# Kernel optimization log

Measured on AMD Instinct MI355X. Metric: run time of the kernel, lower is better.

## Reference

```python
import jax, jax.numpy as jnp
import numpy as np

NUM_LANDMARKS = 256
PINV_ITERS = 6


def iterative_inv(K):
    # Newton-Schulz iterative pseudo-inverse (Nystromformer), K: [B, m, m]
    I = jnp.eye(K.shape[-1], dtype=K.dtype)
    V = K.swapaxes(-1, -2) / (jnp.max(jnp.sum(K, axis=-2)) * jnp.max(jnp.sum(K, axis=-1)))
    for _ in range(PINV_ITERS):
        KV = K @ V
        V = 0.25 * V @ (13.0 * I - KV @ (15.0 * I - KV @ (7.0 * I - KV)))
    return V


def nystrom_attention_matrix(q, k, m):
    # q, k: [B, N, d] -> approximate softmax(q k^T / sqrt(d)) of shape [B, N, N]
    B, N, d = q.shape
    scale = 1.0 / jnp.sqrt(jnp.asarray(d, q.dtype))
    L = N // m
    q_l = q.reshape(B, m, L, d).mean(axis=2)  # landmark queries [B, m, d]
    k_l = k.reshape(B, m, L, d).mean(axis=2)  # landmark keys    [B, m, d]
    k1 = jax.nn.softmax(jnp.einsum('bnd,bmd->bnm', q, k_l) * scale, axis=-1)   # [B, N, m]
    k2 = jax.nn.softmax(jnp.einsum('bld,bmd->blm', q_l, k_l) * scale, axis=-1) # [B, m, m]
    k3 = jax.nn.softmax(jnp.einsum('bmd,bnd->bmn', q_l, k) * scale, axis=-1)   # [B, m, N]
    return (k1 @ iterative_inv(k2)) @ k3  # [B, N, N]


def setup_inputs() -> dict:
    key = jax.random.key(0)
    ks = jax.random.split(key, 8)
    B, C, T, W, H = 2, 64, 4, 32, 32
    d = C // 8
    scale = 0.05  # keep q.k scores in a sane softmax range
    return {
        'x': jax.random.normal(ks[0], (B, C, T, W, H), dtype=jnp.float32),
        'wq': jax.random.normal(ks[1], (d, C), dtype=jnp.float32) * scale,
        'bq': jax.random.normal(ks[2], (d,), dtype=jnp.float32) * scale,
        'wk': jax.random.normal(ks[3], (d, C), dtype=jnp.float32) * scale,
        'bk': jax.random.normal(ks[4], (d,), dtype=jnp.float32) * scale,
        'wv': jax.random.normal(ks[5], (C, C), dtype=jnp.float32) * scale,
        'bv': jax.random.normal(ks[6], (C,), dtype=jnp.float32) * scale,
        'gamma': jax.random.normal(ks[7], (1,), dtype=jnp.float32),
    }


def reference(x, wq, bq, wk, bk, wv, bv, gamma):
    B, C, T, W, H = x.shape
    N = T * W * H
    xf = x.reshape(B, C, N)
    # 1x1x1 Conv3d == per-token linear over channels
    q = jnp.einsum('oc,bcn->bno', wq, xf) + bq            # [B, N, C//8]
    k = jnp.einsum('oc,bcn->bno', wk, xf) + bk            # [B, N, C//8]
    v = jnp.einsum('oc,bcn->bon', wv, xf) + bv[None, :, None]  # [B, C, N]
    attn = nystrom_attention_matrix(q, k, NUM_LANDMARKS)  # [B, N, N]
    # out = bmm(value, attn^T): out[b,c,i] = sum_j v[b,c,j] * attn[b,i,j]
    out = jnp.einsum('bcj,bij->bci', v, attn).reshape(B, C, T, W, H)
    out = gamma[0] * out + x
    return out, attn
```

## Files before the change

### kernel.cpp

```cpp
#include <hip/hip_runtime.h>
#include <hip/hip_bf16.h>
#include <math.h>

#define NB 2
#define NC 64
#define ND 8
#define NN 4096
#define NM 256
#define NL 16
#define SCALE 0.35355339059327373f
#define A_ROOT 4.1303956f
#define B_COEF (-2.8696044f)
#define C_COEF 3.1474086f

typedef __attribute__((ext_vector_type(4))) float f32x4;
typedef __attribute__((ext_vector_type(8))) short bf16x8;
typedef __attribute__((ext_vector_type(4))) short bf16x4;

__device__ inline ushort f2bf(float f) {
  __hip_bfloat16 h = __float2bfloat16(f);
  return *reinterpret_cast<ushort*>(&h);
}
__device__ inline float bf2f(ushort u) {
  return __uint_as_float(((unsigned int)u) << 16);
}

__device__ inline void gl_lds16(const void* g, void* l) {
  __builtin_amdgcn_global_load_lds(
      (const __attribute__((address_space(1))) unsigned int*)g,
      (__attribute__((address_space(3))) unsigned int*)l, 16, 0, 0);
}

__device__ inline unsigned lds_addr(const void* p) {
  return (unsigned)(size_t)(__attribute__((address_space(3))) const void*)p;
}

__global__ __launch_bounds__(256) void qkv2_kernel(
    const float* __restrict__ x,
    const float* __restrict__ wq, const float* __restrict__ bq,
    const float* __restrict__ wk, const float* __restrict__ bk,
    const float* __restrict__ wv, const float* __restrict__ bv,
    float* __restrict__ q, float* __restrict__ k, float* __restrict__ v) {
  __shared__ float ws[NC];
  int o = blockIdx.x;
  int b = blockIdx.z;
  int n0 = blockIdx.y * 1024;
  int t = threadIdx.x;
  const float* wrow;
  float bias;
  if (o < ND)            { wrow = wq + (size_t)o * NC;            bias = bq[o]; }
  else if (o < 2 * ND)   { wrow = wk + (size_t)(o - ND) * NC;     bias = bk[o - ND]; }
  else                   { wrow = wv + (size_t)(o - 2 * ND) * NC; bias = bv[o - 2 * ND]; }
  if (t < NC) ws[t] = wrow[t];
  __syncthreads();
  int n = n0 + t * 4;
  float4 acc = {bias, bias, bias, bias};
  #pragma unroll
  for (int c = 0; c < NC; ++c) {
    float wc = ws[c];
    float4 xv = *(const float4*)(x + ((size_t)b * NC + c) * NN + n);
    acc.x += wc * xv.x; acc.y += wc * xv.y; acc.z += wc * xv.z; acc.w += wc * xv.w;
  }
  if (o < ND) {
    float* qp = q + ((size_t)b * NN + n) * ND + o;
    qp[0] = acc.x; qp[8] = acc.y; qp[16] = acc.z; qp[24] = acc.w;
  } else if (o < 2 * ND) {
    float* kp = k + ((size_t)b * NN + n) * ND + (o - ND);
    kp[0] = acc.x; kp[8] = acc.y; kp[16] = acc.z; kp[24] = acc.w;
  } else {
    *(float4*)(v + ((size_t)b * NC + (o - 2 * ND)) * NN + n) = acc;
  }
}

__global__ void landmark_kernel(const float* __restrict__ q, const float* __restrict__ k,
                                float* __restrict__ ql, float* __restrict__ kl) {
  int idx = blockIdx.x * 256 + threadIdx.x;
  int b = idx / (NM * ND), r = idx % (NM * ND), i = r / ND, o = r % ND;
  float sq = 0.f, sk = 0.f;
  for (int l = 0; l < NL; ++l) {
    size_t base = ((size_t)b * NN + i * NL + l) * ND + o;
    sq += q[base]; sk += k[base];
  }
  ql[idx] = sq * (1.0f / NL);
  kl[idx] = sk * (1.0f / NL);
}

__global__ __launch_bounds__(256) void scores_softmax_m_bf16(
    const float* __restrict__ Q, int R, const float* __restrict__ KL,
    ushort* __restrict__ out) {
  __shared__ float skl[NM][9];
  int b = blockIdx.y;
  int t = threadIdx.x;
  for (int i = t; i < NM * ND; i += 256) skl[i >> 3][i & 7] = KL[(size_t)b * NM * ND + i];
  __syncthreads();
  int wave = t >> 6, lane = t & 63;
  int r = blockIdx.x * 4 + wave;
  const float* qrow = Q + ((size_t)b * R + r) * ND;
  float qr[ND];
  #pragma unroll
  for (int dd = 0; dd < ND; ++dd) qr[dd] = qrow[dd];
  float sc[4];
  float lmax = -1e30f;
  #pragma unroll
  for (int s = 0; s < 4; ++s) {
    int j = lane + 64 * s;
    float a = 0.f;
    #pragma unroll
    for (int dd = 0; dd < ND; ++dd) a += qr[dd] * skl[j][dd];
    sc[s] = a * SCALE;
    lmax = fmaxf(lmax, sc[s]);
  }
  for (int off = 32; off; off >>= 1) lmax = fmaxf(lmax, __shfl_xor(lmax, off));
  float lsum = 0.f;
  #pragma unroll
  for (int s = 0; s < 4; ++s) { sc[s] = expf(sc[s] - lmax); lsum += sc[s]; }
  for (int off = 32; off; off >>= 1) lsum += __shfl_xor(lsum, off);
  float inv = 1.0f / lsum;
  #pragma unroll
  for (int s = 0; s < 4; ++s)
    out[((size_t)b * R + r) * NM + lane + 64 * s] = f2bf(sc[s] * inv);
}

__global__ __launch_bounds__(256) void scores_softmax_m_f32(
    const float* __restrict__ Q, int R, const float* __restrict__ KL,
    float* __restrict__ out) {
  __shared__ float skl[NM][9];
  int b = blockIdx.y;
  int t = threadIdx.x;
  for (int i = t; i < NM * ND; i += 256) skl[i >> 3][i & 7] = KL[(size_t)b * NM * ND + i];
  __syncthreads();
  int wave = t >> 6, lane = t & 63;
  int r = blockIdx.x * 4 + wave;
  const float* qrow = Q + ((size_t)b * R + r) * ND;
  float qr[ND];
  #pragma unroll
  for (int dd = 0; dd < ND; ++dd) qr[dd] = qrow[dd];
  float sc[4];
  float lmax = -1e30f;
  #pragma unroll
  for (int s = 0; s < 4; ++s) {
    int j = lane + 64 * s;
    float a = 0.f;
    #pragma unroll
    for (int dd = 0; dd < ND; ++dd) a += qr[dd] * skl[j][dd];
    sc[s] = a * SCALE;
    lmax = fmaxf(lmax, sc[s]);
  }
  for (int off = 32; off; off >>= 1) lmax = fmaxf(lmax, __shfl_xor(lmax, off));
  float lsum = 0.f;
  #pragma unroll
  for (int s = 0; s < 4; ++s) { sc[s] = expf(sc[s] - lmax); lsum += sc[s]; }
  for (int off = 32; off; off >>= 1) lsum += __shfl_xor(lsum, off);
  float inv = 1.0f / lsum;
  #pragma unroll
  for (int s = 0; s < 4; ++s) out[((size_t)b * R + r) * NM + lane + 64 * s] = sc[s] * inv;
}

__global__ __launch_bounds__(256) void scores_softmax_n(
    const float* __restrict__ QL, const float* __restrict__ Kt,
    ushort* __restrict__ out) {
  __shared__ float wred[4], wsum[4];
  int b = blockIdx.y, i = blockIdx.x;
  int t = threadIdx.x;
  float qr[ND];
  #pragma unroll
  for (int dd = 0; dd < ND; ++dd) qr[dd] = QL[((size_t)b * NM + i) * ND + dd];
  float sc[16];
  float lmax = -1e30f;
  #pragma unroll
  for (int s = 0; s < 16; ++s) {
    int n = t + 256 * s;
    const float* kp = Kt + ((size_t)b * NN + n) * ND;
    float a = 0.f;
    #pragma unroll
    for (int dd = 0; dd < ND; ++dd) a += qr[dd] * kp[dd];
    sc[s] = a * SCALE;
    lmax = fmaxf(lmax, sc[s]);
  }
  for (int off = 32; off; off >>= 1) lmax = fmaxf(lmax, __shfl_xor(lmax, off));
  if ((t & 63) == 0) wred[t >> 6] = lmax;
  __syncthreads();
  lmax = fmaxf(fmaxf(wred[0], wred[1]), fmaxf(wred[2], wred[3]));
  float lsum = 0.f;
  #pragma unroll
  for (int s = 0; s < 16; ++s) { sc[s] = expf(sc[s] - lmax); lsum += sc[s]; }
  for (int off = 32; off; off >>= 1) lsum += __shfl_xor(lsum, off);
  if ((t & 63) == 0) wsum[t >> 6] = lsum;
  __syncthreads();
  lsum = wsum[0] + wsum[1] + wsum[2] + wsum[3];
  float inv = 1.0f / lsum;
  #pragma unroll
  for (int s = 0; s < 16; ++s)
    out[((size_t)b * NM + i) * NN + t + 256 * s] = f2bf(sc[s] * inv);
}

__global__ __launch_bounds__(256) void denom_kernel(const float* __restrict__ k2,
                                                    float* __restrict__ denw) {
  __shared__ float red[256];
  int b = blockIdx.x;
  int t = threadIdx.x;
  float cs = 0.f;
  for (int i = 0; i < NM; ++i) cs += k2[((size_t)b * NM + i) * NM + t];
  red[t] = cs;
  __syncthreads();
  for (int off = 128; off; off >>= 1) {
    if (t < off) red[t] = fmaxf(red[t], red[t + off]);
    __syncthreads();
  }
  if (t == 0) denw[b] = red[0];
}

__global__ void vinit_kernel(const float* __restrict__ k2, const float* __restrict__ denw,
                             float* __restrict__ V) {
  int idx = blockIdx.x * 256 + threadIdx.x;
  int b = idx / (NM * NM), r = idx % (NM * NM), i = r / NM, j = r % NM;
  float dval = 1.0f / fmaxf(denw[0], denw[1]);
  V[idx] = k2[((size_t)b * NM + j) * NM + i] * dval;
}

#define NS_SMEM 70144

__device__ __forceinline__ void ns_tile(
    const float* __restrict__ A, const float* __restrict__ B,
    const float* __restrict__ B2, float* __restrict__ O,
    float s_a, float s_ab, size_t bo, int bi, int bj, char* smem, int t) {
  typedef float ARow[260];
  typedef float BRow[36];
  ARow* As = (ARow*)smem;
  BRow* Bs = (BRow*)(smem + 33280);
  #pragma unroll
  for (int q = 0; q < 8; ++q) {
    int s = q * 256 + t;
    int ar = s >> 6, ac = (s & 63) * 4;
    *(float4*)&As[ar][ac] = *(const float4*)(A + bo + (size_t)(bi + ar) * NM + ac);
    int bk = s >> 3, bc = (s & 7) * 4;
    if (B2 == nullptr) {
      *(float4*)&Bs[bk][bc] = *(const float4*)(B + bo + (size_t)bk * NM + bj + bc);
    } else {
      float4 v = *(const float4*)(B + bo + (size_t)bk * NM + bj + bc);
      float4 z = *(const float4*)(B2 + bo + (size_t)bk * NM + bj + bc);
      float4 rr;
      rr.x = v.x + B_COEF * z.x; rr.y = v.y + B_COEF * z.y;
      rr.z = v.z + B_COEF * z.z; rr.w = v.w + B_COEF * z.w;
      int d = bk - bj - bc;
      if (d >= 0 && d < 4) ((float*)&rr)[d] += C_COEF;
      *(float4*)&Bs[bk][bc] = rr;
    }
  }
  __syncthreads();
  int tx = t & 15, ty = t >> 4;
  float acc[2][2] = {};
  #pragma unroll 8
  for (int kk = 0; kk < NM; ++kk) {
    float a0 = As[ty * 2][kk], a1 = As[ty * 2 + 1][kk];
    float b0 = Bs[kk][tx * 2], b1 = Bs[kk][tx * 2 + 1];
    acc[0][0] += a0 * b0; acc[0][1] += a0 * b1;
    acc[1][0] += a1 * b0; acc[1][1] += a1 * b1;
  }
  #pragma unroll
  for (int i = 0; i < 2; ++i)
    #pragma unroll
    for (int j = 0; j < 2; ++j) {
      size_t o = bo + (size_t)(bi + ty * 2 + i) * NM + bj + tx * 2 + j;
      float r = s_ab * acc[i][j];
      if (s_a != 0.0f) r += s_a * A[o];
      O[o] = r;
    }
}

__global__ __launch_bounds__(256) void ns_z_kernel(
    const float* __restrict__ k2, const float* __restrict__ V, float* __restrict__ Z) {
  __shared__ char smem[NS_SMEM];
  int blk = blockIdx.x, t = threadIdx.x;
  int b = blk >> 6, tile = blk & 63;
  int bi = (tile >> 3) * 32, bj = (tile & 7) * 32;
  ns_tile(k2, V, nullptr, Z, 0.f, 1.f, (size_t)b * NM * NM, bi, bj, smem, t);
}

__global__ __launch_bounds__(256) void ns_uz2_kernel(
    const float* __restrict__ V, const float* __restrict__ Z,
    float* __restrict__ U, float* __restrict__ Z2) {
  __shared__ char smem[NS_SMEM];
  int blk = blockIdx.x, t = threadIdx.x;
  if (blk < NB * 64) {
    int b = blk >> 6, tile = blk & 63;
    int bi = (tile >> 3) * 32, bj = (tile & 7) * 32;
    ns_tile(V, Z, nullptr, U, -A_ROOT, 1.f, (size_t)b * NM * NM, bi, bj, smem, t);
  } else {
    int r = blk - NB * 64;
    int b = r >> 6, tile = r & 63;
    int bi = (tile >> 3) * 32, bj = (tile & 7) * 32;
    ns_tile(Z, Z, nullptr, Z2, 0.f, 1.f, (size_t)b * NM * NM, bi, bj, smem, t);
  }
}

__global__ __launch_bounds__(256) void ns_v_kernel(
    const float* __restrict__ U, const float* __restrict__ Z2,
    const float* __restrict__ Z, float* __restrict__ Vout) {
  __shared__ char smem[NS_SMEM];
  int blk = blockIdx.x, t = threadIdx.x;
  int b = blk >> 6, tile = blk & 63;
  int bi = (tile >> 3) * 32, bj = (tile & 7) * 32;
  ns_tile(U, Z2, Z, Vout, 0.f, -0.25f, (size_t)b * NM * NM, bi, bj, smem, t);
}

__global__ __launch_bounds__(256) void cvt_vinv_kernel(const float* __restrict__ Va,
                                                       ushort* __restrict__ Vt) {
  int b = blockIdx.z;
  int n0 = blockIdx.x * 32, m0 = blockIdx.y * 32;
  __shared__ float tile[32][33];
  int t = threadIdx.x;
  int r = t >> 3, c4 = (t & 7) * 4;
  float4 v = *(const float4*)(Va + ((size_t)b * NM + m0 + r) * NM + n0 + c4);
  tile[c4][r] = v.x; tile[c4 + 1][r] = v.y; tile[c4 + 2][r] = v.z; tile[c4 + 3][r] = v.w;
  __syncthreads();
  ushort4 u;
  u.x = f2bf(tile[r][c4]);     u.y = f2bf(tile[r][c4 + 1]);
  u.z = f2bf(tile[r][c4 + 2]); u.w = f2bf(tile[r][c4 + 3]);
  *(ushort4*)(Vt + ((size_t)b * NM + n0 + r) * NM + m0 + c4) = u;
}

__global__ __launch_bounds__(256) void gemm_a_mfma(
    const ushort* __restrict__ k1bf, const ushort* __restrict__ Vt,
    ushort* __restrict__ Abf) {
  int b = blockIdx.z;
  int bi = blockIdx.y * 128, bj = blockIdx.x * 128;
  __shared__ ushort As[128 * 64];
  __shared__ ushort Bs[128 * 64];
  int t = threadIdx.x;
  int wave = t >> 6, lane = t & 63;
  int wr = wave >> 1, wc = wave & 1;
  const ushort* Ab = k1bf + (size_t)b * NN * NM;
  const ushort* Bb = Vt + (size_t)b * NM * NM;
  f32x4 acc[4][4] = {};
  for (int k0 = 0; k0 < NM; k0 += 64) {
    #pragma unroll
    for (int q = 0; q < 4; ++q) {
      int s = q * 256 + t;
      int r = s >> 3, c = s & 7;
      int cs = (c ^ (r & 7)) << 3;
      gl_lds16(Ab + (size_t)(bi + r) * NM + k0 + cs, As + (size_t)s * 8);
      gl_lds16(Bb + (size_t)(bj + r) * NM + k0 + cs, Bs + (size_t)s * 8);
    }
    __syncthreads();
    #pragma unroll
    for (int kk = 0; kk < 2; ++kk) {
      int koff = kk * 64 + (lane >> 4) * 16;
      bf16x8 af[4], bfv[4];
      #pragma unroll
      for (int mi = 0; mi < 4; ++mi) {
        int row = wr * 64 + mi * 16 + (lane & 15);
        af[mi] = *(const bf16x8*)((const char*)As + row * 128 + (koff ^ ((row & 7) << 4)));
      }
      #pragma unroll
      for (int nj = 0; nj < 4; ++nj) {
        int row = wc * 64 + nj * 16 + (lane & 15);
        bfv[nj] = *(const bf16x8*)((const char*)Bs + row * 128 + (koff ^ ((row & 7) << 4)));
      }
      #pragma unroll
      for (int mi = 0; mi < 4; ++mi)
        #pragma unroll
        for (int nj = 0; nj < 4; ++nj)
          acc[mi][nj] = __builtin_amdgcn_mfma_f32_16x16x32_bf16(af[mi], bfv[nj], acc[mi][nj], 0, 0, 0);
    }
    __syncthreads();
  }
  int col = lane & 15, rbase = (lane >> 4) * 4;
  #pragma unroll
  for (int mi = 0; mi < 4; ++mi)
    #pragma unroll
    for (int nj = 0; nj < 4; ++nj)
      #pragma unroll
      for (int r = 0; r < 4; ++r)
        Abf[((size_t)b * NN + bi + wr * 64 + mi * 16 + rbase + r) * NM
            + bj + wc * 64 + nj * 16 + col] = f2bf(acc[mi][nj][r]);
}

__global__ __launch_bounds__(256) void gemm_attn_mfma(
    const ushort* __restrict__ Abf, const ushort* __restrict__ k3bf,
    float* __restrict__ attn) {
  int lin = blockIdx.z * 1024 + blockIdx.y * 32 + blockIdx.x;
  int swz = (lin & 7) * 256 + (lin >> 3);
  int b = swz >> 10;
  int rem = swz & 1023;
  int bi = (rem >> 5) * 128, bj = (rem & 31) * 128;
  __shared__ ushort As[128 * 64];
  __shared__ ushort Bs[8 * 64 * 16];
  int t = threadIdx.x;
  int wave = t >> 6, lane = t & 63;
  int wr = wave >> 1, wc = wave & 1;
  const ushort* Ab = Abf + (size_t)b * NN * NM;
  const ushort* Bb = k3bf + (size_t)b * NM * NN;
  f32x4 acc[4][4] = {};
  unsigned bs_base = lds_addr(&Bs[0]);
  unsigned trlane = (unsigned)((lane & 15) * 2 + (lane >> 4) * 256);
  for (int k0 = 0; k0 < NM; k0 += 64) {
    #pragma unroll
    for (int q = 0; q < 4; ++q) {
      int s = q * 256 + t;
      int r = s >> 3, c = s & 7;
      int cs = (c ^ (r & 7)) << 3;
      gl_lds16(Ab + (size_t)(bi + r) * NM + k0 + cs, As + (size_t)s * 8);
      int cq = s >> 7, kk2 = (s >> 1) & 63, hf = s & 1;
      gl_lds16(Bb + (size_t)(k0 + kk2) * NN + bj + cq * 16 + hf * 8,
               Bs + (size_t)s * 8);
    }
    __syncthreads();
    #pragma unroll
    for (int kk = 0; kk < 2; ++kk) {
      int koff = kk * 64 + (lane >> 4) * 16;
      bf16x8 af[4], bfv[4];
      #pragma unroll
      for (int mi = 0; mi < 4; ++mi) {
        int row = wr * 64 + mi * 16 + (lane & 15);
        af[mi] = *(const bf16x8*)((const char*)As + row * 128 + (koff ^ ((row & 7) << 4)));
      }
      #pragma unroll
      for (int nj = 0; nj < 4; ++nj) {
        int cq = wc * 4 + nj;
        unsigned a32 = bs_base + (unsigned)(cq * 2048 + kk * 1024) + trlane;
        bf16x4 lo, hi;
        asm volatile("ds_read_b64_tr_b16 %0, %2 offset:0\n\t"
                     "ds_read_b64_tr_b16 %1, %2 offset:128"
                     : "=&v"(lo), "=&v"(hi) : "v"(a32));
        bfv[nj] = __builtin_shufflevector(lo, hi, 0, 1, 2, 3, 4, 5, 6, 7);
      }
      asm volatile("s_waitcnt lgkmcnt(0)" ::: "memory");
      __builtin_amdgcn_sched_barrier(0);
      #pragma unroll
      for (int mi = 0; mi < 4; ++mi)
        #pragma unroll
        for (int nj = 0; nj < 4; ++nj)
          acc[mi][nj] = __builtin_amdgcn_mfma_f32_16x16x32_bf16(af[mi], bfv[nj], acc[mi][nj], 0, 0, 0);
    }
    __syncthreads();
  }
  int col = lane & 15, rbase = (lane >> 4) * 4;
  #pragma unroll
  for (int mi = 0; mi < 4; ++mi)
    #pragma unroll
    for (int nj = 0; nj < 4; ++nj)
      #pragma unroll
      for (int r = 0; r < 4; ++r)
        attn[((size_t)b * NN + bi + wr * 64 + mi * 16 + rbase + r) * NN
             + bj + wc * 64 + nj * 16 + col] = acc[mi][nj][r];
}

__global__ __launch_bounds__(256) void kv_kernel(
    const ushort* __restrict__ K3, const float* __restrict__ Vv,
    float* __restrict__ kvout) {
  int b = blockIdx.z, bp = blockIdx.x * 64;
  int j0base = blockIdx.y * (NN / 32);
  __shared__ float Ks[64][33], Vs[64][33];
  int t = threadIdx.x, tx = t & 15, ty = t >> 4;
  int lrow = t >> 2, ljc = (t & 3) * 8;
  float acc[4][4] = {};
  for (int j0 = j0base; j0 < j0base + NN / 32; j0 += 32) {
    bf16x8 a0 = *(const bf16x8*)(K3 + ((size_t)b * NM + bp + lrow) * NN + j0 + ljc);
    float4 v0 = *(const float4*)(Vv + ((size_t)b * NC + lrow) * NN + j0 + ljc);
    float4 v1 = *(const float4*)(Vv + ((size_t)b * NC + lrow) * NN + j0 + ljc + 4);
    #pragma unroll
    for (int e = 0; e < 8; ++e) Ks[lrow][ljc + e] = bf2f((ushort)a0[e]);
    Vs[lrow][ljc + 0] = v0.x; Vs[lrow][ljc + 1] = v0.y; Vs[lrow][ljc + 2] = v0.z; Vs[lrow][ljc + 3] = v0.w;
    Vs[lrow][ljc + 4] = v1.x; Vs[lrow][ljc + 5] = v1.y; Vs[lrow][ljc + 6] = v1.z; Vs[lrow][ljc + 7] = v1.w;
    __syncthreads();
    #pragma unroll
    for (int kk = 0; kk < 32; ++kk) {
      float av_[4], bv_[4];
      #pragma unroll
      for (int i = 0; i < 4; ++i) av_[i] = Ks[(ty << 2) + i][kk];
      #pragma unroll
      for (int j = 0; j < 4; ++j) bv_[j] = Vs[(tx << 2) + j][kk];
      #pragma unroll
      for (int i = 0; i < 4; ++i)
        #pragma unroll
        for (int j = 0; j < 4; ++j) acc[i][j] += av_[i] * bv_[j];
    }
    __syncthreads();
  }
  #pragma unroll
  for (int i = 0; i < 4; ++i)
    #pragma unroll
    for (int j = 0; j < 4; ++j)
      atomicAdd(&kvout[((size_t)b * NM + bp + (ty << 2) + i) * NC + (tx << 2) + j], acc[i][j]);
}

__global__ __launch_bounds__(256) void out_kernel(
    const ushort* __restrict__ Abf, const float* __restrict__ kvm,
    const float* __restrict__ x, const float* __restrict__ gamma,
    float* __restrict__ outp) {
  __shared__ float As[32 * 256];
  int blk = blockIdx.x;
  int b = blk / (NN / 32), n0 = (blk % (NN / 32)) * 32;
  int t = threadIdx.x;
  for (int it = 0; it < 32; ++it)
    As[it * 256 + (t ^ (it & 31))] = bf2f(Abf[((size_t)b * NN + n0 + it) * NM + t]);
  __syncthreads();
  int tn = t & 31, cg0 = (t >> 5) * 8;
  float g = gamma[0];
  float acc[8] = {};
  for (int p = 0; p < NM; ++p) {
    float a = As[tn * 256 + (p ^ (tn & 31))];
    float4 kv0 = *(const float4*)(kvm + ((size_t)b * NM + p) * NC + cg0);
    float4 kv1 = *(const float4*)(kvm + ((size_t)b * NM + p) * NC + cg0 + 4);
    acc[0] += a * kv0.x; acc[1] += a * kv0.y; acc[2] += a * kv0.z; acc[3] += a * kv0.w;
    acc[4] += a * kv1.x; acc[5] += a * kv1.y; acc[6] += a * kv1.z; acc[7] += a * kv1.w;
  }
  #pragma unroll
  for (int qd = 0; qd < 8; ++qd) {
    int c = cg0 + qd;
    size_t idx = ((size_t)b * NC + c) * NN + n0 + tn;
    outp[idx] = g * acc[qd] + x[idx];
  }
}

extern "C" void kernel_launch(void* const* d_in, const int* in_sizes, int n_in,
                              void* d_out, int out_size, void* d_ws, size_t ws_size,
                              hipStream_t stream) {
  const float* x     = (const float*)d_in[0];
  const float* wq    = (const float*)d_in[1];
  const float* bq    = (const float*)d_in[2];
  const float* wk    = (const float*)d_in[3];
  const float* bk    = (const float*)d_in[4];
  const float* wv    = (const float*)d_in[5];
  const float* bv    = (const float*)d_in[6];
  const float* gamma = (const float*)d_in[7];
  float* outp = (float*)d_out;
  float* attn = outp + (size_t)NB * NC * NN;
  float* w = (float*)d_ws;

  float* qw   = w;
  float* kw   = qw + 65536;
  float* vw   = kw + 65536;
  float* qlw  = vw + 524288;
  float* klw  = qlw + 4096;
  float* k1w  = klw + 4096;
  float* k2w  = k1w + 2097152;
  float* spare= k2w + 131072;
  float* Abuf = spare + 2097152;
  float* Zb   = Abuf + 1048576;
  float* Z2b  = Zb + 131072;
  float* Ub   = Z2b + 131072;
  float* Va   = Ub + 131072;
  float* Vtw  = Va + 131072;
  float* kvw  = Vtw + 65536;
  float* denw = kvw + 32768;
  ushort* k1bf  = (ushort*)k1w;
  ushort* k3bf  = (ushort*)k1w + 2097152;
  ushort* Abf   = (ushort*)Abuf;
  ushort* Vinvt = (ushort*)Vtw;

  hipMemsetAsync(kvw, 0, (size_t)NB * NM * NC * sizeof(float), stream);
  qkv2_kernel<<<dim3(80, NN / 1024, NB), dim3(256), 0, stream>>>(
      x, wq, bq, wk, bk, wv, bv, qw, kw, vw);
  landmark_kernel<<<dim3(NB * NM * ND / 256), dim3(256), 0, stream>>>(qw, kw, qlw, klw);
  scores_softmax_m_bf16<<<dim3(NN / 4, NB), dim3(256), 0, stream>>>(qw, NN, klw, k1bf);
  scores_softmax_m_f32<<<dim3(NM / 4, NB), dim3(256), 0, stream>>>(qlw, NM, klw, k2w);
  scores_softmax_n<<<dim3(NM, NB), dim3(256), 0, stream>>>(qlw, kw, k3bf);
  denom_kernel<<<dim3(NB), dim3(256), 0, stream>>>(k2w, denw);
  vinit_kernel<<<dim3(NB * NM * NM / 256), dim3(256), 0, stream>>>(k2w, denw, Va);

  for (int it = 0; it < 6; ++it) {
    ns_z_kernel<<<dim3(NB * 64), dim3(256), 0, stream>>>(k2w, Va, Zb);
    ns_uz2_kernel<<<dim3(2 * NB * 64), dim3(256), 0, stream>>>(Va, Zb, Ub, Z2b);
    ns_v_kernel<<<dim3(NB * 64), dim3(256), 0, stream>>>(Ub, Z2b, Zb, Va);
  }

  cvt_vinv_kernel<<<dim3(NM / 32, NM / 32, NB), dim3(256), 0, stream>>>(Va, Vinvt);
  gemm_a_mfma<<<dim3(NM / 128, NN / 128, NB), dim3(256), 0, stream>>>(k1bf, Vinvt, Abf);
  gemm_attn_mfma<<<dim3(NN / 128, NN / 128, NB), dim3(256), 0, stream>>>(Abf, k3bf, attn);
  kv_kernel<<<dim3(NM / 64, 32, NB), dim3(256), 0, stream>>>(k3bf, vw, kvw);
  out_kernel<<<dim3(NB * NN / 32), dim3(256), 0, stream>>>(Abf, kvw, x, gamma, outp);
}
```

Measured before the change: 317.9 us.

## Drop transpose LDS reads; pre-transpose k3 to bf16 N-major layout

The attention GEMM previously loaded k3 in bf16 [m,N] layout and used ds_read_b64_tr_b16 transpose reads from LDS. Now scores_softmax_n writes fp32 k3, a new cvt_t_kernel transposes it into a bf16 [N,m] buffer, and the GEMM loads B with the same swizzled row layout as A. kv_kernel now reads fp32 k3 directly. This adds an extra kernel launch and extra fp32 traffic (a larger k3 write plus the transpose pass) in exchange for simpler, conventional LDS reads in the GEMM.

```diff
diff --git a/kernel.cpp b/kernel.cpp
--- a/kernel.cpp
+++ b/kernel.cpp
@@ -15,7 +15,6 @@
 
 typedef __attribute__((ext_vector_type(4))) float f32x4;
 typedef __attribute__((ext_vector_type(8))) short bf16x8;
-typedef __attribute__((ext_vector_type(4))) short bf16x4;
 
 __device__ inline ushort f2bf(float f) {
   __hip_bfloat16 h = __float2bfloat16(f);
@@ -29,10 +28,6 @@
   __builtin_amdgcn_global_load_lds(
       (const __attribute__((address_space(1))) unsigned int*)g,
       (__attribute__((address_space(3))) unsigned int*)l, 16, 0, 0);
-}
-
-__device__ inline unsigned lds_addr(const void* p) {
-  return (unsigned)(size_t)(__attribute__((address_space(3))) const void*)p;
 }
 
 __global__ __launch_bounds__(256) void qkv2_kernel(
@@ -158,7 +153,7 @@
 
 __global__ __launch_bounds__(256) void scores_softmax_n(
     const float* __restrict__ QL, const float* __restrict__ Kt,
-    ushort* __restrict__ out) {
+    float* __restrict__ out) {
   __shared__ float wred[4], wsum[4];
   int b = blockIdx.y, i = blockIdx.x;
   int t = threadIdx.x;
@@ -190,8 +185,7 @@
   lsum = wsum[0] + wsum[1] + wsum[2] + wsum[3];
   float inv = 1.0f / lsum;
   #pragma unroll
-  for (int s = 0; s < 16; ++s)
-    out[((size_t)b * NM + i) * NN + t + 256 * s] = f2bf(sc[s] * inv);
+  for (int s = 0; s < 16; ++s) out[((size_t)b * NM + i) * NN + t + 256 * s] = sc[s] * inv;
 }
 
 __global__ __launch_bounds__(256) void denom_kernel(const float* __restrict__ k2,
@@ -320,6 +314,22 @@
   *(ushort4*)(Vt + ((size_t)b * NM + n0 + r) * NM + m0 + c4) = u;
 }
 
+__global__ __launch_bounds__(256) void cvt_t_kernel(const float* __restrict__ k3,
+                                                    ushort* __restrict__ k3t) {
+  int b = blockIdx.z;
+  int n0 = blockIdx.x * 32, m0 = blockIdx.y * 32;
+  __shared__ float tile[32][33];
+  int t = threadIdx.x;
+  int r = t >> 3, c4 = (t & 7) * 4;
+  float4 v = *(const float4*)(k3 + ((size_t)b * NM + m0 + r) * NN + n0 + c4);
+  tile[c4][r] = v.x; tile[c4 + 1][r] = v.y; tile[c4 + 2][r] = v.z; tile[c4 + 3][r] = v.w;
+  __syncthreads();
+  ushort4 u;
+  u.x = f2bf(tile[r][c4]);     u.y = f2bf(tile[r][c4 + 1]);
+  u.z = f2bf(tile[r][c4 + 2]); u.w = f2bf(tile[r][c4 + 3]);
+  *(ushort4*)(k3t + ((size_t)b * NN + n0 + r) * NM + m0 + c4) = u;
+}
+
 __global__ __launch_bounds__(256) void gemm_a_mfma(
     const ushort* __restrict__ k1bf, const ushort* __restrict__ Vt,
     ushort* __restrict__ Abf) {
@@ -377,7 +387,7 @@
 }
 
 __global__ __launch_bounds__(256) void gemm_attn_mfma(
-    const ushort* __restrict__ Abf, const ushort* __restrict__ k3bf,
+    const ushort* __restrict__ Abf, const ushort* __restrict__ K3T,
     float* __restrict__ attn) {
   int lin = blockIdx.z * 1024 + blockIdx.y * 32 + blockIdx.x;
   int swz = (lin & 7) * 256 + (lin >> 3);
@@ -385,15 +395,13 @@
   int rem = swz & 1023;
   int bi = (rem >> 5) * 128, bj = (rem & 31) * 128;
   __shared__ ushort As[128 * 64];
-  __shared__ ushort Bs[8 * 64 * 16];
+  __shared__ ushort Bs[128 * 64];
   int t = threadIdx.x;
   int wave = t >> 6, lane = t & 63;
   int wr = wave >> 1, wc = wave & 1;
   const ushort* Ab = Abf + (size_t)b * NN * NM;
-  const ushort* Bb = k3bf + (size_t)b * NM * NN;
+  const ushort* Bb = K3T + (size_t)b * NN * NM;
   f32x4 acc[4][4] = {};
-  unsigned bs_base = lds_addr(&Bs[0]);
-  unsigned trlane = (unsigned)((lane & 15) * 2 + (lane >> 4) * 256);
   for (int k0 = 0; k0 < NM; k0 += 64) {
     #pragma unroll
     for (int q = 0; q < 4; ++q) {
@@ -401,9 +409,7 @@
       int r = s >> 3, c = s & 7;
       int cs = (c ^ (r & 7)) << 3;
       gl_lds16(Ab + (size_t)(bi + r) * NM + k0 + cs, As + (size_t)s * 8);
-      int cq = s >> 7, kk2 = (s >> 1) & 63, hf = s & 1;
-      gl_lds16(Bb + (size_t)(k0 + kk2) * NN + bj + cq * 16 + hf * 8,
-               Bs + (size_t)s * 8);
+      gl_lds16(Bb + (size_t)(bj + r) * NM + k0 + cs, Bs + (size_t)s * 8);
     }
     __syncthreads();
     #pragma unroll
@@ -417,16 +423,9 @@
       }
       #pragma unroll
       for (int nj = 0; nj < 4; ++nj) {
-        int cq = wc * 4 + nj;
-        unsigned a32 = bs_base + (unsigned)(cq * 2048 + kk * 1024) + trlane;
-        bf16x4 lo, hi;
-        asm volatile("ds_read_b64_tr_b16 %0, %2 offset:0\n\t"
-                     "ds_read_b64_tr_b16 %1, %2 offset:128"
-                     : "=&v"(lo), "=&v"(hi) : "v"(a32));
-        bfv[nj] = __builtin_shufflevector(lo, hi, 0, 1, 2, 3, 4, 5, 6, 7);
+        int row = wc * 64 + nj * 16 + (lane & 15);
+        bfv[nj] = *(const bf16x8*)((const char*)Bs + row * 128 + (koff ^ ((row & 7) << 4)));
       }
-      asm volatile("s_waitcnt lgkmcnt(0)" ::: "memory");
-      __builtin_amdgcn_sched_barrier(0);
       #pragma unroll
       for (int mi = 0; mi < 4; ++mi)
         #pragma unroll
@@ -447,7 +446,7 @@
 }
 
 __global__ __launch_bounds__(256) void kv_kernel(
-    const ushort* __restrict__ K3, const float* __restrict__ Vv,
+    const float* __restrict__ K3, const float* __restrict__ Vv,
     float* __restrict__ kvout) {
   int b = blockIdx.z, bp = blockIdx.x * 64;
   int j0base = blockIdx.y * (NN / 32);
@@ -456,11 +455,12 @@
   int lrow = t >> 2, ljc = (t & 3) * 8;
   float acc[4][4] = {};
   for (int j0 = j0base; j0 < j0base + NN / 32; j0 += 32) {
-    bf16x8 a0 = *(const bf16x8*)(K3 + ((size_t)b * NM + bp + lrow) * NN + j0 + ljc);
+    float4 a0 = *(const float4*)(K3 + ((size_t)b * NM + bp + lrow) * NN + j0 + ljc);
+    float4 a1 = *(const float4*)(K3 + ((size_t)b * NM + bp + lrow) * NN + j0 + ljc + 4);
     float4 v0 = *(const float4*)(Vv + ((size_t)b * NC + lrow) * NN + j0 + ljc);
     float4 v1 = *(const float4*)(Vv + ((size_t)b * NC + lrow) * NN + j0 + ljc + 4);
-    #pragma unroll
-    for (int e = 0; e < 8; ++e) Ks[lrow][ljc + e] = bf2f((ushort)a0[e]);
+    Ks[lrow][ljc + 0] = a0.x; Ks[lrow][ljc + 1] = a0.y; Ks[lrow][ljc + 2] = a0.z; Ks[lrow][ljc + 3] = a0.w;
+    Ks[lrow][ljc + 4] = a1.x; Ks[lrow][ljc + 5] = a1.y; Ks[lrow][ljc + 6] = a1.z; Ks[lrow][ljc + 7] = a1.w;
     Vs[lrow][ljc + 0] = v0.x; Vs[lrow][ljc + 1] = v0.y; Vs[lrow][ljc + 2] = v0.z; Vs[lrow][ljc + 3] = v0.w;
     Vs[lrow][ljc + 4] = v1.x; Vs[lrow][ljc + 5] = v1.y; Vs[lrow][ljc + 6] = v1.z; Vs[lrow][ljc + 7] = v1.w;
     __syncthreads();
@@ -536,8 +536,8 @@
   float* klw  = qlw + 4096;
   float* k1w  = klw + 4096;
   float* k2w  = k1w + 2097152;
-  float* spare= k2w + 131072;
-  float* Abuf = spare + 2097152;
+  float* k3w  = k2w + 131072;
+  float* Abuf = k3w + 2097152;
   float* Zb   = Abuf + 1048576;
   float* Z2b  = Zb + 131072;
   float* Ub   = Z2b + 131072;
@@ -546,7 +546,7 @@
   float* kvw  = Vtw + 65536;
   float* denw = kvw + 32768;
   ushort* k1bf  = (ushort*)k1w;
-  ushort* k3bf  = (ushort*)k1w + 2097152;
+  ushort* k3T   = (ushort*)k1w + 2097152;
   ushort* Abf   = (ushort*)Abuf;
   ushort* Vinvt = (ushort*)Vtw;
 
@@ -556,7 +556,7 @@
   landmark_kernel<<<dim3(NB * NM * ND / 256), dim3(256), 0, stream>>>(qw, kw, qlw, klw);
   scores_softmax_m_bf16<<<dim3(NN / 4, NB), dim3(256), 0, stream>>>(qw, NN, klw, k1bf);
   scores_softmax_m_f32<<<dim3(NM / 4, NB), dim3(256), 0, stream>>>(qlw, NM, klw, k2w);
-  scores_softmax_n<<<dim3(NM, NB), dim3(256), 0, stream>>>(qlw, kw, k3bf);
+  scores_softmax_n<<<dim3(NM, NB), dim3(256), 0, stream>>>(qlw, kw, k3w);
   denom_kernel<<<dim3(NB), dim3(256), 0, stream>>>(k2w, denw);
   vinit_kernel<<<dim3(NB * NM * NM / 256), dim3(256), 0, stream>>>(k2w, denw, Va);
 
@@ -567,8 +567,9 @@
   }
 
   cvt_vinv_kernel<<<dim3(NM / 32, NM / 32, NB), dim3(256), 0, stream>>>(Va, Vinvt);
+  cvt_t_kernel<<<dim3(NN / 32, NM / 32, NB), dim3(256), 0, stream>>>(k3w, k3T);
   gemm_a_mfma<<<dim3(NM / 128, NN / 128, NB), dim3(256), 0, stream>>>(k1bf, Vinvt, Abf);
-  gemm_attn_mfma<<<dim3(NN / 128, NN / 128, NB), dim3(256), 0, stream>>>(Abf, k3bf, attn);
-  kv_kernel<<<dim3(NM / 64, 32, NB), dim3(256), 0, stream>>>(k3bf, vw, kvw);
+  gemm_attn_mfma<<<dim3(NN / 128, NN / 128, NB), dim3(256), 0, stream>>>(Abf, k3T, attn);
+  kv_kernel<<<dim3(NM / 64, 32, NB), dim3(256), 0, stream>>>(k3w, vw, kvw);
   out_kernel<<<dim3(NB * NN / 32), dim3(256), 0, stream>>>(Abf, kvw, x, gamma, outp);
 }
```

After: 319.0 us. Within noise of the previous version (+0.3%).
